# Performance work log

Hardware: AMD Instinct MI355X
Metric: run time of the kernel (lower is better)

The kernel has to match this reference:

```python
import jax, jax.numpy as jnp
import numpy as np

EPS = 0.0  # torch .norm division has no eps; keep exact

def setup_inputs() -> dict:
    key = jax.random.key(0)
    B, T, C = 32, 1024, 768
    x = jax.random.normal(key, (B, T, C), dtype=jnp.float32)
    return {"x": x}

def reference(x) -> jnp.ndarray:
    # Faithful device-side math of Block_ATC.forward -> agglomerative_clustering:
    #   metric = x / ||x||_2 (last dim); scores = metric @ metric^T; dist = 1 - scores
    # The subsequent scipy linkage/fcluster runs on CPU per-batch and its results
    # are discarded in the original code (labels stay zeros, forward returns None),
    # so the cosine-distance matrix is the meaningful computed tensor.
    metric = x / jnp.linalg.norm(x, axis=-1, keepdims=True)  # [B,T,C]
    scores = jnp.einsum('btc,bsc->bts', metric, metric)      # [B,T,T]
    return 1.0 - scores
```

## Files before the change

kernel.cpp:

```cpp
#include <hip/hip_runtime.h>
#include <hip/hip_bf16.h>
#include <stdint.h>

#define B_DIM 32
#define T_DIM 1024
#define C_DIM 768

typedef __bf16 bf16x8 __attribute__((ext_vector_type(8)));
typedef float f32x4 __attribute__((ext_vector_type(4)));

typedef __attribute__((address_space(1))) void gvoid_t;
typedef __attribute__((address_space(3))) void lvoid_t;

__device__ __forceinline__ unsigned short f32_to_bf16_rne(float f) {
    union { float f; uint32_t u; } v; v.f = f;
    uint32_t u = v.u;
    uint32_t r = 0x7fffu + ((u >> 16) & 1u);
    return (unsigned short)((u + r) >> 16);
}

__global__ __launch_bounds__(256) void normalize_rows(const float* __restrict__ x,
                                                      unsigned short* __restrict__ m) {
    const int row  = blockIdx.x * 4 + (threadIdx.x >> 6);
    const int lane = threadIdx.x & 63;
    const float4* xr = (const float4*)(x + (size_t)row * C_DIM);
    float4 v0 = xr[lane];
    float4 v1 = xr[lane + 64];
    float4 v2 = xr[lane + 128];
    float ss = v0.x*v0.x + v0.y*v0.y + v0.z*v0.z + v0.w*v0.w
             + v1.x*v1.x + v1.y*v1.y + v1.z*v1.z + v1.w*v1.w
             + v2.x*v2.x + v2.y*v2.y + v2.z*v2.z + v2.w*v2.w;
    #pragma unroll
    for (int off = 32; off > 0; off >>= 1)
        ss += __shfl_xor(ss, off, 64);
    const float rs = rsqrtf(ss);
    ushort4* mr = (ushort4*)(m + (size_t)row * C_DIM);
    ushort4 o;
    o.x = f32_to_bf16_rne(v0.x * rs); o.y = f32_to_bf16_rne(v0.y * rs);
    o.z = f32_to_bf16_rne(v0.z * rs); o.w = f32_to_bf16_rne(v0.w * rs);
    mr[lane] = o;
    o.x = f32_to_bf16_rne(v1.x * rs); o.y = f32_to_bf16_rne(v1.y * rs);
    o.z = f32_to_bf16_rne(v1.z * rs); o.w = f32_to_bf16_rne(v1.w * rs);
    mr[lane + 64] = o;
    o.x = f32_to_bf16_rne(v2.x * rs); o.y = f32_to_bf16_rne(v2.y * rs);
    o.z = f32_to_bf16_rne(v2.z * rs); o.w = f32_to_bf16_rne(v2.w * rs);
    mr[lane + 128] = o;
}

__global__ __launch_bounds__(256) void gemm_nt(const unsigned short* __restrict__ M,
                                               float* __restrict__ out) {
    __shared__ unsigned short As[128 * 32];
    __shared__ unsigned short Bs[128 * 32];

    const int b  = blockIdx.z;
    const int ti = blockIdx.y;
    const int tj = blockIdx.x;

    const int tid  = threadIdx.x;
    const int wave = tid >> 6;
    const int lane = tid & 63;
    const int quad = lane >> 4;
    const int l16  = lane & 15;
    const int wi = wave >> 1;
    const int wj = wave & 1;

    const unsigned short* Mb = M + (size_t)b * T_DIM * C_DIM;

    const int srow0 = (wave * 2 + 0) * 16 + (lane >> 2);
    const int srow1 = (wave * 2 + 1) * 16 + (lane >> 2);
    const int scol  = (lane & 3) * 8;

    const unsigned short* gA0 = Mb + (size_t)(ti * 128 + srow0) * C_DIM + scol;
    const unsigned short* gA1 = Mb + (size_t)(ti * 128 + srow1) * C_DIM + scol;
    const unsigned short* gB0 = Mb + (size_t)(tj * 128 + srow0) * C_DIM + scol;
    const unsigned short* gB1 = Mb + (size_t)(tj * 128 + srow1) * C_DIM + scol;

    unsigned short* lA0 = &As[(wave * 2 + 0) * 512];
    unsigned short* lA1 = &As[(wave * 2 + 1) * 512];
    unsigned short* lB0 = &Bs[(wave * 2 + 0) * 512];
    unsigned short* lB1 = &Bs[(wave * 2 + 1) * 512];

    f32x4 acc[4][4];
    #pragma unroll
    for (int i = 0; i < 4; ++i)
        #pragma unroll
        for (int j = 0; j < 4; ++j)
            acc[i][j] = (f32x4){0.f, 0.f, 0.f, 0.f};

    for (int k0 = 0; k0 < C_DIM; k0 += 32) {
        __builtin_amdgcn_global_load_lds((gvoid_t*)(gA0 + k0), (lvoid_t*)lA0, 16, 0, 0);
        __builtin_amdgcn_global_load_lds((gvoid_t*)(gA1 + k0), (lvoid_t*)lA1, 16, 0, 0);
        __builtin_amdgcn_global_load_lds((gvoid_t*)(gB0 + k0), (lvoid_t*)lB0, 16, 0, 0);
        __builtin_amdgcn_global_load_lds((gvoid_t*)(gB1 + k0), (lvoid_t*)lB1, 16, 0, 0);
        __syncthreads();

        bf16x8 af[4], bfr[4];
        #pragma unroll
        for (int ii = 0; ii < 4; ++ii) {
            af[ii]  = *(const bf16x8*)&As[(wi * 64 + ii * 16 + l16) * 32 + quad * 8];
            bfr[ii] = *(const bf16x8*)&Bs[(wj * 64 + ii * 16 + l16) * 32 + quad * 8];
        }
        #pragma unroll
        for (int ii = 0; ii < 4; ++ii)
            #pragma unroll
            for (int jj = 0; jj < 4; ++jj)
                acc[ii][jj] = __builtin_amdgcn_mfma_f32_16x16x32_bf16(af[ii], bfr[jj], acc[ii][jj], 0, 0, 0);
        __syncthreads();
    }

    float* outb = out + (size_t)b * T_DIM * T_DIM;
    #pragma unroll
    for (int ii = 0; ii < 4; ++ii) {
        const int rowbase = ti * 128 + wi * 64 + ii * 16 + quad * 4;
        #pragma unroll
        for (int jj = 0; jj < 4; ++jj) {
            const int col = tj * 128 + wj * 64 + jj * 16 + l16;
            #pragma unroll
            for (int r = 0; r < 4; ++r)
                outb[(size_t)(rowbase + r) * T_DIM + col] = 1.0f - acc[ii][jj][r];
        }
    }
}

extern "C" void kernel_launch(void* const* d_in, const int* in_sizes, int n_in,
                              void* d_out, int out_size, void* d_ws, size_t ws_size,
                              hipStream_t stream) {
    const float* x = (const float*)d_in[0];
    float* out = (float*)d_out;
    unsigned short* metric = (unsigned short*)d_ws;

    normalize_rows<<<dim3((B_DIM * T_DIM) / 4), dim3(256), 0, stream>>>(x, metric);
    gemm_nt<<<dim3(T_DIM / 128, T_DIM / 128, B_DIM), dim3(256), 0, stream>>>(metric, out);
}
```

Baseline: 277.4 us.

## Exploit Gram matrix symmetry: compute upper-triangular tiles and mirror-store

```diff
diff --git a/kernel.cpp b/kernel.cpp
--- a/kernel.cpp
+++ b/kernel.cpp
@@ -1,10 +1,13 @@
 #include <hip/hip_runtime.h>
 #include <hip/hip_bf16.h>
 #include <stdint.h>
+#include <math.h>
 
 #define B_DIM 32
 #define T_DIM 1024
 #define C_DIM 768
+#define NTILE 8
+#define NTRI  36
 
 typedef __bf16 bf16x8 __attribute__((ext_vector_type(8)));
 typedef float f32x4 __attribute__((ext_vector_type(4)));
@@ -47,14 +50,16 @@
     mr[lane + 128] = o;
 }
 
-__global__ __launch_bounds__(256) void gemm_nt(const unsigned short* __restrict__ M,
-                                               float* __restrict__ out) {
+__global__ __launch_bounds__(256) void gemm_nt_sym(const unsigned short* __restrict__ M,
+                                                   float* __restrict__ out) {
     __shared__ unsigned short As[128 * 32];
     __shared__ unsigned short Bs[128 * 32];
 
-    const int b  = blockIdx.z;
-    const int ti = blockIdx.y;
-    const int tj = blockIdx.x;
+    const int b   = blockIdx.y;
+    const int idx = blockIdx.x;
+    int tj = (int)((sqrtf(8.0f * (float)idx + 1.0f) - 1.0f) * 0.5f);
+    if (tj * (tj + 1) / 2 > idx) --tj;
+    const int ti = idx - tj * (tj + 1) / 2;
 
     const int tid  = threadIdx.x;
     const int wave = tid >> 6;
@@ -120,6 +125,22 @@
                 outb[(size_t)(rowbase + r) * T_DIM + col] = 1.0f - acc[ii][jj][r];
         }
     }
+    if (ti != tj) {
+        #pragma unroll
+        for (int ii = 0; ii < 4; ++ii) {
+            const int rowbase = ti * 128 + wi * 64 + ii * 16 + quad * 4;
+            #pragma unroll
+            for (int jj = 0; jj < 4; ++jj) {
+                const int col = tj * 128 + wj * 64 + jj * 16 + l16;
+                f32x4 v;
+                v[0] = 1.0f - acc[ii][jj][0];
+                v[1] = 1.0f - acc[ii][jj][1];
+                v[2] = 1.0f - acc[ii][jj][2];
+                v[3] = 1.0f - acc[ii][jj][3];
+                *(f32x4*)(outb + (size_t)col * T_DIM + rowbase) = v;
+            }
+        }
+    }
 }
 
 extern "C" void kernel_launch(void* const* d_in, const int* in_sizes, int n_in,
@@ -130,5 +151,5 @@
     unsigned short* metric = (unsigned short*)d_ws;
 
     normalize_rows<<<dim3((B_DIM * T_DIM) / 4), dim3(256), 0, stream>>>(x, metric);
-    gemm_nt<<<dim3(T_DIM / 128, T_DIM / 128, B_DIM), dim3(256), 0, stream>>>(metric, out);
+    gemm_nt_sym<<<dim3(NTRI, B_DIM), dim3(256), 0, stream>>>(metric, out);
 }
```

Result: slower. 283.4 us (+2.2%).
